# Kernel optimization log

Measured on AMD Instinct MI355X. Metric: run time of the kernel, lower is better.

Reference implementation:

```python
import jax, jax.numpy as jnp
import numpy as np

DEPTH = 4      # truncation depth of the signature
DIM = 8        # path channels
PATH_LEN = 16384
STREAM = True


def _restricted_exp(z, depth):
    # exp(z) in truncated tensor algebra: level k term = z^{\otimes k}/k!, flattened to [d**k]
    terms = [z]
    for k in range(2, depth + 1):
        terms.append((terms[-1][:, None] * z[None, :]).reshape(-1) / k)
    return tuple(terms)


def _chen_mult(a, b, depth):
    # Truncated tensor-algebra product (Chen's relation); a_0 = b_0 = 1 implicit.
    # c_k = a_k + b_k + sum_{i=1}^{k-1} a_i \otimes b_{k-i}
    c = []
    for k in range(depth):
        t = a[k] + b[k]
        for i in range(k):
            t = t + (a[i][:, None] * b[k - 1 - i][None, :]).reshape(-1)
        c.append(t)
    return tuple(c)


def setup_inputs() -> dict:
    key = jax.random.key(0)
    path = jax.random.normal(key, (PATH_LEN, DIM), dtype=jnp.float32)
    return {"path": path}


def reference(path):
    depth = DEPTH
    d = path.shape[-1]
    inc = path[1:] - path[:-1]                                # [N-1, d] increments
    exps = jax.vmap(lambda z: _restricted_exp(z, depth))(inc)  # tuple of [N-1, d**k]
    init = tuple(jnp.zeros((d ** (k + 1),), dtype=path.dtype) for k in range(depth))

    def step(carry, x):
        new = _chen_mult(carry, x, depth)
        return new, (new if STREAM else None)

    last, ys = jax.lax.scan(step, init, exps)
    if STREAM:
        # flatten: concat levels -> [N-1, d + d^2 + ... + d^depth]
        return jnp.concatenate([y for y in ys], axis=-1)
    return jnp.concatenate(last, axis=-1)
```

## Files before the change

kernel.cpp:

```cpp
#include <hip/hip_runtime.h>

#define NPATH 16384
#define DIM   8
#define NINC  (NPATH - 1)
#define SIG   4680
#define L1OFF 0
#define L2OFF 8
#define L3OFF 72
#define L4OFF 584
#define NCHUNK 256
#define CHUNK  64
#define NSUB  2048
#define SUB   8
#define NGRP  16
#define GSIZE 16
#define C6    0.16666666666666666f
#define LPAD  17


__device__ __forceinline__ void light_barrier() {
  asm volatile("s_waitcnt lgkmcnt(0)" ::: "memory");
  __builtin_amdgcn_s_barrier();
}

__device__ __forceinline__ void zero_state(float r4[16], float r3[2],
                                           float& a1i, float& a2v,
                                           float& a2s, float& a1s, float& a1t) {
#pragma unroll
  for (int l = 0; l < 16; ++l) r4[l] = 0.f;
  r3[0] = r3[1] = 0.f;
  a1i = a2v = a2s = a1s = a1t = 0.f;
}

__device__ __forceinline__ void store_sig_reg(float* __restrict__ dst,
                                              const float r4[16], const float r3[2],
                                              float a2s, float a1t, int t) {
  float4* d4 = (float4*)(dst + L4OFF + 16 * t);
  d4[0] = make_float4(r4[0], r4[1], r4[2], r4[3]);
  d4[1] = make_float4(r4[4], r4[5], r4[6], r4[7]);
  d4[2] = make_float4(r4[8], r4[9], r4[10], r4[11]);
  d4[3] = make_float4(r4[12], r4[13], r4[14], r4[15]);
  *(float2*)(dst + L3OFF + 2 * t) = make_float2(r3[0], r3[1]);
  if (t < 64) dst[L2OFF + t] = a2s;
  if (t < 8)  dst[L1OFF + t] = a1t;
}

__device__ __forceinline__ void load_state(const float* __restrict__ src,
                                           float r4[16], float r3[2],
                                           float& a1i, float& a2v,
                                           float& a2s, float& a1s, float& a1t, int t) {
  const float4* s4 = (const float4*)(src + L4OFF + 16 * t);
  float4 G0 = s4[0], G1 = s4[1], G2 = s4[2], G3 = s4[3];
  r4[0]=G0.x; r4[1]=G0.y; r4[2]=G0.z; r4[3]=G0.w;
  r4[4]=G1.x; r4[5]=G1.y; r4[6]=G1.z; r4[7]=G1.w;
  r4[8]=G2.x; r4[9]=G2.y; r4[10]=G2.z; r4[11]=G2.w;
  r4[12]=G3.x; r4[13]=G3.y; r4[14]=G3.z; r4[15]=G3.w;
  const float2 gr3 = *(const float2*)(src + L3OFF + 2 * t);
  r3[0] = gr3.x; r3[1] = gr3.y;
  a1i = src[L1OFF + (t >> 5)];
  a2v = src[L2OFF + (t >> 2)];
  a2s = a1s = a1t = 0.f;
  if (t < 64) { a2s = src[L2OFF + t]; a1s = src[L1OFF + (t >> 3)]; }
  if (t < 8)  { a1t = src[L1OFF + t]; }
}

struct ChenB {
  float4 B0, B1, B2, B3;
  float4 C0, C1, C2, C3;
  float4 D0, D1, D2, D3;
  float4 E0, E1;
  float2 b3c, b2jk, b1k;
  float  b2ij, b1j, b1i, b2t, b1j2, b1i2, b1t;
};

__device__ __forceinline__ void chen_load(const float* __restrict__ b, int t, ChenB& R) {
  const int i   = t >> 5;
  const int j   = (t >> 2) & 7;
  const int ij  = t >> 2;
  const int c0  = 2 * t;
  const int jk0 = c0 & 63;
  const int k0  = 2 * (t & 3);
  const int i2  = t >> 3;
  const int j2  = t & 7;
  const float4* bv = (const float4*)b;
  R.B0 = bv[146 + 4 * t]; R.B1 = bv[147 + 4 * t]; R.B2 = bv[148 + 4 * t]; R.B3 = bv[149 + 4 * t];
  R.C0 = bv[18 + 2 * jk0]; R.C1 = bv[19 + 2 * jk0]; R.C2 = bv[20 + 2 * jk0]; R.C3 = bv[21 + 2 * jk0];
  R.D0 = bv[2 + 2 * k0]; R.D1 = bv[3 + 2 * k0]; R.D2 = bv[4 + 2 * k0]; R.D3 = bv[5 + 2 * k0];
  R.E0 = bv[0]; R.E1 = bv[1];
  R.b3c  = *(const float2*)(b + L3OFF + c0);
  R.b2jk = *(const float2*)(b + L2OFF + jk0);
  R.b1k  = *(const float2*)(b + L1OFF + k0);
  R.b2ij = b[L2OFF + ij];
  R.b1j  = b[L1OFF + j];
  R.b1i  = b[L1OFF + i];
  R.b2t = 0.f; R.b1j2 = 0.f; R.b1i2 = 0.f; R.b1t = 0.f;
  if (t < 64) { R.b2t = b[L2OFF + t]; R.b1j2 = b[L1OFF + j2]; R.b1i2 = b[L1OFF + i2]; }
  if (t < 8)  { R.b1t = b[L1OFF + t]; }
}

__device__ __forceinline__ void chen_apply(float r4[16], float r3[2],
                                           float& a1i, float& a2v,
                                           float& a2s, float& a1s, float& a1t,
                                           const ChenB& R, int t) {
  const float b4r[16] = {R.B0.x,R.B0.y,R.B0.z,R.B0.w, R.B1.x,R.B1.y,R.B1.z,R.B1.w,
                         R.B2.x,R.B2.y,R.B2.z,R.B2.w, R.B3.x,R.B3.y,R.B3.z,R.B3.w};
  const float b3r[16] = {R.C0.x,R.C0.y,R.C0.z,R.C0.w, R.C1.x,R.C1.y,R.C1.z,R.C1.w,
                         R.C2.x,R.C2.y,R.C2.z,R.C2.w, R.C3.x,R.C3.y,R.C3.z,R.C3.w};
  const float b2r[16] = {R.D0.x,R.D0.y,R.D0.z,R.D0.w, R.D1.x,R.D1.y,R.D1.z,R.D1.w,
                         R.D2.x,R.D2.y,R.D2.z,R.D2.w, R.D3.x,R.D3.y,R.D3.z,R.D3.w};
  const float b1r[8]  = {R.E0.x,R.E0.y,R.E0.z,R.E0.w, R.E1.x,R.E1.y,R.E1.z,R.E1.w};
#pragma unroll
  for (int l = 0; l < 8; ++l) {
    r4[l]     += b4r[l]     + a1i * b3r[l]     + a2v * b2r[l]     + r3[0] * b1r[l];
    r4[8 + l] += b4r[8 + l] + a1i * b3r[8 + l] + a2v * b2r[8 + l] + r3[1] * b1r[l];
  }
  r3[0] += R.b3c.x + a1i * R.b2jk.x + a2v * R.b1k.x;
  r3[1] += R.b3c.y + a1i * R.b2jk.y + a2v * R.b1k.y;
  const float a1i_old = a1i;
  a2v += R.b2ij + a1i_old * R.b1j;
  if (t < 64) { a2s += R.b2t + a1s * R.b1j2; a1s += R.b1i2; }
  a1i = a1i_old + R.b1i;
  if (t < 8) a1t += R.b1t;
}

__device__ __forceinline__ void step_update(const float* zs,
                                            float r4[16], float r3[2],
                                            float& a1i, float& a2v,
                                            float& a2s, float& a1s, float& a1t, int t) {
  const int i  = t >> 5;
  const int j  = (t >> 2) & 7;
  const int k0 = 2 * (t & 3);
  const int i2 = t >> 3;
  const int j2 = t & 7;
  const float zi = zs[i];
  const float zj = zs[j];
  const float2 zk = *(const float2*)(zs + k0);
  const float4 za = *(const float4*)zs;
  const float4 zb = *(const float4*)(zs + 4);
  const float zn[8] = {za.x, za.y, za.z, za.w, zb.x, zb.y, zb.z, zb.w};
  const float a1zi4 = a1i + 0.25f * zi;
  const float zj6   = C6 * zj;
  const float T0 = r3[0] + a2v * (0.5f * zk.x) + a1zi4 * (zj6 * zk.x);
  const float T1 = r3[1] + a2v * (0.5f * zk.y) + a1zi4 * (zj6 * zk.y);
  const float U  = a2v + (0.5f * a1i + C6 * zi) * zj;
#pragma unroll
  for (int l = 0; l < 8; ++l) {
    r4[l]     += T0 * zn[l];
    r4[8 + l] += T1 * zn[l];
  }
  r3[0] += zk.x * U;
  r3[1] += zk.y * U;
  a2v += (a1i + 0.5f * zi) * zj;
  a1i += zi;
  if (t < 64) {
    const float zi2 = zs[i2], zj2v = zs[j2];
    a2s += (a1s + 0.5f * zi2) * zj2v;
    a1s += zi2;
  }
  if (t < 8) a1t += zs[t];
}

__global__ __launch_bounds__(256) void k_totals(const float* __restrict__ path,
                                                float* __restrict__ T64,
                                                float* __restrict__ snap) {
  __shared__ float zbuf[CHUNK][8];
  const int t = threadIdx.x;
  const int b = blockIdx.x;
  const int base = b * CHUNK;
  for (int u = t; u < CHUNK * 8; u += 256) {
    const int s = u >> 3, l = u & 7;
    const int rB = min(base + s + 1, NPATH - 1);
    zbuf[s][l] = path[rB * DIM + l] - path[(base + s) * DIM + l];
  }
  float r4[16], r3[2], a1i, a2v, a2s, a1s, a1t;
  zero_state(r4, r3, a1i, a2v, a2s, a1s, a1t);
  __syncthreads();
  for (int w = 0; w < 8; ++w) {
    store_sig_reg(snap + ((size_t)b * 8 + w) * SIG, r4, r3, a2s, a1t, t);
#pragma unroll
    for (int s2 = 0; s2 < 8; ++s2)
      step_update(zbuf[8 * w + s2], r4, r3, a1i, a2v, a2s, a1s, a1t, t);
  }
  store_sig_reg(T64 + (size_t)b * SIG, r4, r3, a2s, a1t, t);
}

__global__ __launch_bounds__(256) void k_scan(const float* __restrict__ in,
                                              float* __restrict__ prefout,
                                              float* __restrict__ totout,
                                              int count) {
  const int t = threadIdx.x;
  const size_t goff = (size_t)blockIdx.x * count;
  float r4[16], r3[2], a1i, a2v, a2s, a1s, a1t;
  zero_state(r4, r3, a1i, a2v, a2s, a1s, a1t);
  ChenB bA, bB;
  chen_load(in + goff * SIG, t, bA);
  for (int m = 0; m < count; m += 2) {
    if (m + 1 < count) chen_load(in + (goff + m + 1) * SIG, t, bB);
    store_sig_reg(prefout + (goff + m) * SIG, r4, r3, a2s, a1t, t);
    chen_apply(r4, r3, a1i, a2v, a2s, a1s, a1t, bA, t);
    if (m + 1 >= count) break;
    if (m + 2 < count) chen_load(in + (goff + m + 2) * SIG, t, bA);
    store_sig_reg(prefout + (goff + m + 1) * SIG, r4, r3, a2s, a1t, t);
    chen_apply(r4, r3, a1i, a2v, a2s, a1s, a1t, bB, t);
  }
  if (totout != nullptr) store_sig_reg(totout + (size_t)blockIdx.x * SIG, r4, r3, a2s, a1t, t);
}

__global__ __launch_bounds__(256) void k_states(const float* __restrict__ pref,
                                                const float* __restrict__ gpref,
                                                const float* __restrict__ snap,
                                                float* __restrict__ states) {
  const int t = threadIdx.x;
  const int sIdx = blockIdx.x;
  const int b = sIdx >> 3;
  const int g = b >> 4;
  float r4[16], r3[2], a1i, a2v, a2s, a1s, a1t;
  ChenB cA, cB;
  chen_load(pref + (size_t)b * SIG, t, cA);
  chen_load(snap + (size_t)sIdx * SIG, t, cB);
  load_state(gpref + (size_t)g * SIG, r4, r3, a1i, a2v, a2s, a1s, a1t, t);
  chen_apply(r4, r3, a1i, a2v, a2s, a1s, a1t, cA, t);
  chen_apply(r4, r3, a1i, a2v, a2s, a1s, a1t, cB, t);
  store_sig_reg(states + (size_t)sIdx * SIG, r4, r3, a2s, a1t, t);
}

__global__ __launch_bounds__(256, 8) void k_stream(const float* __restrict__ path,
                                                   const float* __restrict__ states,
                                                   float* __restrict__ out) {
  __shared__ float zbuf[SUB][8];
  __shared__ __align__(16) float lbuf[256 * LPAD];
  const int t = threadIdx.x;
  const int sIdx = blockIdx.x;
  const int base = sIdx * SUB;
  const int n = min(SUB, NINC - base);
  if (t < SUB * 8) {
    const int s = t >> 3, l = t & 7;
    const int rB = min(base + s + 1, NPATH - 1);
    zbuf[s][l] = path[rB * DIM + l] - path[(base + s) * DIM + l];
  }
  float r4[16], r3[2], a1i, a2v, a2s, a1s, a1t;
  load_state(states + (size_t)sIdx * SIG, r4, r3, a1i, a2v, a2s, a1s, a1t, t);
  __syncthreads();
  const int tp = t >> 2;
  const int rq = 4 * (t & 3);
  for (int s2 = 0; s2 < n; ++s2) {
    step_update(zbuf[s2], r4, r3, a1i, a2v, a2s, a1s, a1t, t);
    float* lb = lbuf + LPAD * t;
    *(float4*)(lb + 0)  = make_float4(r4[0], r4[1], r4[2], r4[3]);
    *(float4*)(lb + 4)  = make_float4(r4[4], r4[5], r4[6], r4[7]);
    *(float4*)(lb + 8)  = make_float4(r4[8], r4[9], r4[10], r4[11]);
    *(float4*)(lb + 12) = make_float4(r4[12], r4[13], r4[14], r4[15]);
    light_barrier();
    float* dst = out + (size_t)(base + s2) * SIG;
#pragma unroll
    for (int q = 0; q < 4; ++q) {
      const float4 v = *(const float4*)(lbuf + LPAD * (tp + 64 * q) + rq);
      *(float4*)(dst + L4OFF + 4 * t + 1024 * q) = v;
    }
    *(float2*)(dst + L3OFF + 2 * t) = make_float2(r3[0], r3[1]);
    if (t < 64) dst[L2OFF + t] = a2s;
    if (t < 8)  dst[L1OFF + t] = a1t;
    light_barrier();
  }
}

extern "C" void kernel_launch(void* const* d_in, const int* in_sizes, int n_in,
                              void* d_out, int out_size, void* d_ws, size_t ws_size,
                              hipStream_t stream) {
  (void)in_sizes; (void)n_in; (void)out_size; (void)ws_size;
  const float* path = (const float*)d_in[0];
  float* out = (float*)d_out;
  float* ws = (float*)d_ws;

  float* T64    = ws;
  float* pref   = T64    + (size_t)NCHUNK * SIG;
  float* gtot   = pref   + (size_t)NCHUNK * SIG;
  float* gpref  = gtot   + (size_t)NGRP * SIG;
  float* snap   = gpref  + (size_t)NGRP * SIG;
  float* states = snap   + (size_t)NSUB * SIG;

  k_totals<<<NCHUNK, 256, 0, stream>>>(path, T64, snap);
  k_scan<<<NGRP, 256, 0, stream>>>(T64, pref, gtot, GSIZE);
  k_scan<<<1, 256, 0, stream>>>(gtot, gpref, nullptr, NGRP);
  k_states<<<NSUB, 256, 0, stream>>>(pref, gpref, snap, states);
  k_stream<<<NSUB, 256, 0, stream>>>(path, states, out);
}
```

Before: 165.5 us.

## Fuse state reconstruction into streaming kernel and double sub-chunk length

Removes the separate k_states kernel and its states buffer. The output kernel now rebuilds each block's starting signature itself by applying the group prefix, the chunk prefix and, when needed, a snapshot through a new register-based Chen product. Sub-chunks grow from 8 to 16 steps, which halves the number of snapshots and output blocks. This saves one launch and a global write/read round trip of the states. In exchange each streaming block does more serial steps and extra Chen loads, and the launch-bounds occupancy hint of 8 is dropped.

```diff
diff --git a/kernel.cpp b/kernel.cpp
--- a/kernel.cpp
+++ b/kernel.cpp
@@ -10,8 +10,9 @@
 #define L4OFF 584
 #define NCHUNK 256
 #define CHUNK  64
-#define NSUB  2048
-#define SUB   8
+#define NSUB  1024
+#define SUB   16
+#define SPC   4
 #define NGRP  16
 #define GSIZE 16
 #define C6    0.16666666666666666f
@@ -62,6 +63,55 @@
   a2s = a1s = a1t = 0.f;
   if (t < 64) { a2s = src[L2OFF + t]; a1s = src[L1OFF + (t >> 3)]; }
   if (t < 8)  { a1t = src[L1OFF + t]; }
+}
+
+__device__ __forceinline__ void chen_reg(float r4[16], float r3[2],
+                                         float& a1i, float& a2v,
+                                         float& a2s, float& a1s, float& a1t,
+                                         const float* __restrict__ b, int t) {
+  const int i   = t >> 5;
+  const int j   = (t >> 2) & 7;
+  const int ij  = t >> 2;
+  const int c0  = 2 * t;
+  const int jk0 = c0 & 63;
+  const int k0  = 2 * (t & 3);
+  const int i2  = t >> 3;
+  const int j2  = t & 7;
+  const float4* bv = (const float4*)b;
+  float4 B0 = bv[146 + 4 * t], B1 = bv[147 + 4 * t], B2 = bv[148 + 4 * t], B3 = bv[149 + 4 * t];
+  float4 Cq0 = bv[18 + 2 * jk0], Cq1 = bv[19 + 2 * jk0], Cq2 = bv[20 + 2 * jk0], Cq3 = bv[21 + 2 * jk0];
+  float4 D0 = bv[2 + 2 * k0], D1 = bv[3 + 2 * k0], D2 = bv[4 + 2 * k0], D3 = bv[5 + 2 * k0];
+  float4 E0 = bv[0], E1 = bv[1];
+  const float2 b3c  = *(const float2*)(b + L3OFF + c0);
+  const float2 b2jk = *(const float2*)(b + L2OFF + jk0);
+  const float2 b1k  = *(const float2*)(b + L1OFF + k0);
+  const float b2ij = b[L2OFF + ij];
+  const float b1j  = b[L1OFF + j];
+  const float b1i  = b[L1OFF + i];
+  float b2t = 0.f, b1j2 = 0.f, b1i2 = 0.f, b1t = 0.f;
+  if (t < 64) { b2t = b[L2OFF + t]; b1j2 = b[L1OFF + j2]; b1i2 = b[L1OFF + i2]; }
+  if (t < 8)  { b1t = b[L1OFF + t]; }
+
+  const float b4r[16] = {B0.x,B0.y,B0.z,B0.w, B1.x,B1.y,B1.z,B1.w,
+                         B2.x,B2.y,B2.z,B2.w, B3.x,B3.y,B3.z,B3.w};
+  const float b3r[16] = {Cq0.x,Cq0.y,Cq0.z,Cq0.w, Cq1.x,Cq1.y,Cq1.z,Cq1.w,
+                         Cq2.x,Cq2.y,Cq2.z,Cq2.w, Cq3.x,Cq3.y,Cq3.z,Cq3.w};
+  const float b2r[16] = {D0.x,D0.y,D0.z,D0.w, D1.x,D1.y,D1.z,D1.w,
+                         D2.x,D2.y,D2.z,D2.w, D3.x,D3.y,D3.z,D3.w};
+  const float b1r[8]  = {E0.x,E0.y,E0.z,E0.w, E1.x,E1.y,E1.z,E1.w};
+
+#pragma unroll
+  for (int l = 0; l < 8; ++l) {
+    r4[l]     += b4r[l]     + a1i * b3r[l]     + a2v * b2r[l]     + r3[0] * b1r[l];
+    r4[8 + l] += b4r[8 + l] + a1i * b3r[8 + l] + a2v * b2r[8 + l] + r3[1] * b1r[l];
+  }
+  r3[0] += b3c.x + a1i * b2jk.x + a2v * b1k.x;
+  r3[1] += b3c.y + a1i * b2jk.y + a2v * b1k.y;
+  const float a1i_old = a1i;
+  a2v += b2ij + a1i_old * b1j;
+  if (t < 64) { a2s += b2t + a1s * b1j2; a1s += b1i2; }
+  a1i = a1i_old + b1i;
+  if (t < 8) a1t += b1t;
 }
 
 struct ChenB {
@@ -175,11 +225,11 @@
   float r4[16], r3[2], a1i, a2v, a2s, a1s, a1t;
   zero_state(r4, r3, a1i, a2v, a2s, a1s, a1t);
   __syncthreads();
-  for (int w = 0; w < 8; ++w) {
-    store_sig_reg(snap + ((size_t)b * 8 + w) * SIG, r4, r3, a2s, a1t, t);
-#pragma unroll
-    for (int s2 = 0; s2 < 8; ++s2)
-      step_update(zbuf[8 * w + s2], r4, r3, a1i, a2v, a2s, a1s, a1t, t);
+  for (int w = 0; w < SPC; ++w) {
+    if (w > 0) store_sig_reg(snap + ((size_t)b * SPC + w) * SIG, r4, r3, a2s, a1t, t);
+#pragma unroll
+    for (int s2 = 0; s2 < SUB; ++s2)
+      step_update(zbuf[SUB * w + s2], r4, r3, a1i, a2v, a2s, a1s, a1t, t);
   }
   store_sig_reg(T64 + (size_t)b * SIG, r4, r3, a2s, a1t, t);
 }
@@ -206,40 +256,29 @@
   if (totout != nullptr) store_sig_reg(totout + (size_t)blockIdx.x * SIG, r4, r3, a2s, a1t, t);
 }
 
-__global__ __launch_bounds__(256) void k_states(const float* __restrict__ pref,
-                                                const float* __restrict__ gpref,
-                                                const float* __restrict__ snap,
-                                                float* __restrict__ states) {
-  const int t = threadIdx.x;
-  const int sIdx = blockIdx.x;
-  const int b = sIdx >> 3;
-  const int g = b >> 4;
-  float r4[16], r3[2], a1i, a2v, a2s, a1s, a1t;
-  ChenB cA, cB;
-  chen_load(pref + (size_t)b * SIG, t, cA);
-  chen_load(snap + (size_t)sIdx * SIG, t, cB);
-  load_state(gpref + (size_t)g * SIG, r4, r3, a1i, a2v, a2s, a1s, a1t, t);
-  chen_apply(r4, r3, a1i, a2v, a2s, a1s, a1t, cA, t);
-  chen_apply(r4, r3, a1i, a2v, a2s, a1s, a1t, cB, t);
-  store_sig_reg(states + (size_t)sIdx * SIG, r4, r3, a2s, a1t, t);
-}
-
-__global__ __launch_bounds__(256, 8) void k_stream(const float* __restrict__ path,
-                                                   const float* __restrict__ states,
-                                                   float* __restrict__ out) {
+__global__ __launch_bounds__(256) void k_out(const float* __restrict__ path,
+                                             const float* __restrict__ pref,
+                                             const float* __restrict__ gpref,
+                                             const float* __restrict__ snap,
+                                             float* __restrict__ out) {
   __shared__ float zbuf[SUB][8];
   __shared__ __align__(16) float lbuf[256 * LPAD];
   const int t = threadIdx.x;
   const int sIdx = blockIdx.x;
+  const int b = sIdx >> 2;
+  const int g = b >> 4;
   const int base = sIdx * SUB;
   const int n = min(SUB, NINC - base);
-  if (t < SUB * 8) {
-    const int s = t >> 3, l = t & 7;
+  for (int u = t; u < SUB * 8; u += 256) {
+    const int s = u >> 3, l = u & 7;
     const int rB = min(base + s + 1, NPATH - 1);
     zbuf[s][l] = path[rB * DIM + l] - path[(base + s) * DIM + l];
   }
   float r4[16], r3[2], a1i, a2v, a2s, a1s, a1t;
-  load_state(states + (size_t)sIdx * SIG, r4, r3, a1i, a2v, a2s, a1s, a1t, t);
+  load_state(gpref + (size_t)g * SIG, r4, r3, a1i, a2v, a2s, a1s, a1t, t);
+  chen_reg(r4, r3, a1i, a2v, a2s, a1s, a1t, pref + (size_t)b * SIG, t);
+  if (sIdx & 3)
+    chen_reg(r4, r3, a1i, a2v, a2s, a1s, a1t, snap + (size_t)sIdx * SIG, t);
   __syncthreads();
   const int tp = t >> 2;
   const int rq = 4 * (t & 3);
@@ -277,11 +316,9 @@
   float* gtot   = pref   + (size_t)NCHUNK * SIG;
   float* gpref  = gtot   + (size_t)NGRP * SIG;
   float* snap   = gpref  + (size_t)NGRP * SIG;
-  float* states = snap   + (size_t)NSUB * SIG;
 
   k_totals<<<NCHUNK, 256, 0, stream>>>(path, T64, snap);
   k_scan<<<NGRP, 256, 0, stream>>>(T64, pref, gtot, GSIZE);
   k_scan<<<1, 256, 0, stream>>>(gtot, gpref, nullptr, NGRP);
-  k_states<<<NSUB, 256, 0, stream>>>(pref, gpref, snap, states);
-  k_stream<<<NSUB, 256, 0, stream>>>(path, states, out);
-}
+  k_out<<<NSUB, 256, 0, stream>>>(path, pref, gpref, snap, out);
+}
```

New measurement: 139.1 us. 1.19x faster.

## Fuse state reconstruction into stream kernel and drop group-prefix scan launch

Applied to the files above, without the earlier changes.

Removes the single-block group scan and the k_states kernel. Each output block now rebuilds its starting state by Chen-multiplying the preceding group totals, its chunk prefix and its sub-chunk snapshot in registers. Sub-chunks grow from 8 to 16 steps, and the L4 staging buffer is double-buffered so one barrier per step can be dropped. This cuts two launches and a global round trip of the states array. In exchange, later blocks do up to 17 serial Chen products, and the larger shared buffer plus the loss of the occupancy hint may reduce occupancy.

```diff
diff --git a/kernel.cpp b/kernel.cpp
--- a/kernel.cpp
+++ b/kernel.cpp
@@ -10,8 +10,9 @@
 #define L4OFF 584
 #define NCHUNK 256
 #define CHUNK  64
-#define NSUB  2048
-#define SUB   8
+#define NSUB  1024
+#define SUB   16
+#define SPC   4
 #define NGRP  16
 #define GSIZE 16
 #define C6    0.16666666666666666f
@@ -175,11 +176,11 @@
   float r4[16], r3[2], a1i, a2v, a2s, a1s, a1t;
   zero_state(r4, r3, a1i, a2v, a2s, a1s, a1t);
   __syncthreads();
-  for (int w = 0; w < 8; ++w) {
-    store_sig_reg(snap + ((size_t)b * 8 + w) * SIG, r4, r3, a2s, a1t, t);
-#pragma unroll
-    for (int s2 = 0; s2 < 8; ++s2)
-      step_update(zbuf[8 * w + s2], r4, r3, a1i, a2v, a2s, a1s, a1t, t);
+  for (int w = 0; w < SPC; ++w) {
+    if (w > 0) store_sig_reg(snap + ((size_t)b * SPC + w) * SIG, r4, r3, a2s, a1t, t);
+#pragma unroll
+    for (int s2 = 0; s2 < SUB; ++s2)
+      step_update(zbuf[SUB * w + s2], r4, r3, a1i, a2v, a2s, a1s, a1t, t);
   }
   store_sig_reg(T64 + (size_t)b * SIG, r4, r3, a2s, a1t, t);
 }
@@ -206,31 +207,17 @@
   if (totout != nullptr) store_sig_reg(totout + (size_t)blockIdx.x * SIG, r4, r3, a2s, a1t, t);
 }
 
-__global__ __launch_bounds__(256) void k_states(const float* __restrict__ pref,
-                                                const float* __restrict__ gpref,
-                                                const float* __restrict__ snap,
-                                                float* __restrict__ states) {
+__global__ __launch_bounds__(256) void k_out(const float* __restrict__ path,
+                                             const float* __restrict__ pref,
+                                             const float* __restrict__ GT,
+                                             const float* __restrict__ snap,
+                                             float* __restrict__ out) {
+  __shared__ float zbuf[SUB][8];
+  __shared__ __align__(16) float lbuf[2][256 * LPAD];
   const int t = threadIdx.x;
   const int sIdx = blockIdx.x;
-  const int b = sIdx >> 3;
+  const int b = sIdx >> 2;
   const int g = b >> 4;
-  float r4[16], r3[2], a1i, a2v, a2s, a1s, a1t;
-  ChenB cA, cB;
-  chen_load(pref + (size_t)b * SIG, t, cA);
-  chen_load(snap + (size_t)sIdx * SIG, t, cB);
-  load_state(gpref + (size_t)g * SIG, r4, r3, a1i, a2v, a2s, a1s, a1t, t);
-  chen_apply(r4, r3, a1i, a2v, a2s, a1s, a1t, cA, t);
-  chen_apply(r4, r3, a1i, a2v, a2s, a1s, a1t, cB, t);
-  store_sig_reg(states + (size_t)sIdx * SIG, r4, r3, a2s, a1t, t);
-}
-
-__global__ __launch_bounds__(256, 8) void k_stream(const float* __restrict__ path,
-                                                   const float* __restrict__ states,
-                                                   float* __restrict__ out) {
-  __shared__ float zbuf[SUB][8];
-  __shared__ __align__(16) float lbuf[256 * LPAD];
-  const int t = threadIdx.x;
-  const int sIdx = blockIdx.x;
   const int base = sIdx * SUB;
   const int n = min(SUB, NINC - base);
   if (t < SUB * 8) {
@@ -239,28 +226,42 @@
     zbuf[s][l] = path[rB * DIM + l] - path[(base + s) * DIM + l];
   }
   float r4[16], r3[2], a1i, a2v, a2s, a1s, a1t;
-  load_state(states + (size_t)sIdx * SIG, r4, r3, a1i, a2v, a2s, a1s, a1t, t);
+  zero_state(r4, r3, a1i, a2v, a2s, a1s, a1t);
+  const int cnt = g + 1 + ((sIdx & 3) ? 1 : 0);
+#define PADDR(m) ((m) < g ? GT + (size_t)(m) * SIG \
+                          : ((m) == g ? pref + (size_t)b * SIG : snap + (size_t)sIdx * SIG))
+  ChenB cA, cB;
+  chen_load(PADDR(0), t, cA);
+  for (int m = 0; m < cnt; m += 2) {
+    if (m + 1 < cnt) chen_load(PADDR(m + 1), t, cB);
+    chen_apply(r4, r3, a1i, a2v, a2s, a1s, a1t, cA, t);
+    if (m + 1 >= cnt) break;
+    if (m + 2 < cnt) chen_load(PADDR(m + 2), t, cA);
+    chen_apply(r4, r3, a1i, a2v, a2s, a1s, a1t, cB, t);
+  }
+#undef PADDR
   __syncthreads();
   const int tp = t >> 2;
   const int rq = 4 * (t & 3);
+#pragma unroll 4
   for (int s2 = 0; s2 < n; ++s2) {
     step_update(zbuf[s2], r4, r3, a1i, a2v, a2s, a1s, a1t, t);
-    float* lb = lbuf + LPAD * t;
+    float* lb = lbuf[s2 & 1] + LPAD * t;
     *(float4*)(lb + 0)  = make_float4(r4[0], r4[1], r4[2], r4[3]);
     *(float4*)(lb + 4)  = make_float4(r4[4], r4[5], r4[6], r4[7]);
     *(float4*)(lb + 8)  = make_float4(r4[8], r4[9], r4[10], r4[11]);
     *(float4*)(lb + 12) = make_float4(r4[12], r4[13], r4[14], r4[15]);
     light_barrier();
+    const float* lbr = lbuf[s2 & 1];
     float* dst = out + (size_t)(base + s2) * SIG;
 #pragma unroll
     for (int q = 0; q < 4; ++q) {
-      const float4 v = *(const float4*)(lbuf + LPAD * (tp + 64 * q) + rq);
+      const float4 v = *(const float4*)(lbr + LPAD * (tp + 64 * q) + rq);
       *(float4*)(dst + L4OFF + 4 * t + 1024 * q) = v;
     }
     *(float2*)(dst + L3OFF + 2 * t) = make_float2(r3[0], r3[1]);
     if (t < 64) dst[L2OFF + t] = a2s;
     if (t < 8)  dst[L1OFF + t] = a1t;
-    light_barrier();
   }
 }
 
@@ -274,14 +275,10 @@
 
   float* T64    = ws;
   float* pref   = T64    + (size_t)NCHUNK * SIG;
-  float* gtot   = pref   + (size_t)NCHUNK * SIG;
-  float* gpref  = gtot   + (size_t)NGRP * SIG;
-  float* snap   = gpref  + (size_t)NGRP * SIG;
-  float* states = snap   + (size_t)NSUB * SIG;
+  float* GT     = pref   + (size_t)NCHUNK * SIG;
+  float* snap   = GT     + (size_t)NGRP * SIG;
 
   k_totals<<<NCHUNK, 256, 0, stream>>>(path, T64, snap);
-  k_scan<<<NGRP, 256, 0, stream>>>(T64, pref, gtot, GSIZE);
-  k_scan<<<1, 256, 0, stream>>>(gtot, gpref, nullptr, NGRP);
-  k_states<<<NSUB, 256, 0, stream>>>(pref, gpref, snap, states);
-  k_stream<<<NSUB, 256, 0, stream>>>(path, states, out);
-}
+  k_scan<<<NGRP, 256, 0, stream>>>(T64, pref, GT, GSIZE);
+  k_out<<<NSUB, 256, 0, stream>>>(path, pref, GT, snap, out);
+}
```

Result: faster. 133.5 us (-19.4%).
